# Kernel tuning notes

Measured on AMD Instinct MI355X. Metric: run time of the kernel, lower is better.

## Reference

```python
import jax, jax.numpy as jnp
import numpy as np


def _conv(x, w):
    # 'same'-padded NCHW conv, stride 1, no bias (matches nn.Conv2d(..., padding=k//2, bias=False))
    return jax.lax.conv_general_dilated(x, w, (1, 1), 'SAME',
                                        dimension_numbers=('NCHW', 'OIHW', 'NCHW'))


def setup_inputs() -> dict:
    key = jax.random.key(0)
    ks = jax.random.split(key, 11)
    b, C, H, W = 8, 64, 192, 192
    n_classes, n_space = 2, 8
    return {
        'x': jax.random.normal(ks[0], (b, C, H, W), jnp.float32),
        'class_score': jax.random.normal(ks[1], (b, n_classes, H, W), jnp.float32),
        # to_cspace: Conv2d(1, n_space-1, 3, padding=1)
        'W_cspace': jax.random.normal(ks[2], (n_space - 1, 1, 3, 3), jnp.float32) * 0.1,
        # to_xspace: Conv2d(C, C*n_space, 3, padding=1)
        'W_xspace': jax.random.normal(ks[3], (C * n_space, C, 3, 3), jnp.float32) * 0.02,
        # 1x1 convs stored as squeezed vectors (no bias)
        'W_combine_space': jax.random.normal(ks[4], (n_space,), jnp.float32) * 0.3,  # Conv2d(n_space,1,1)
        'W_cvalue': jax.random.normal(ks[5], (n_space,), jnp.float32) * 0.3,        # Conv2d(1,n_space,1)
        'W_attn': jax.random.normal(ks[6], (n_space,), jnp.float32) * 0.3,          # Conv2d(1,n_space,1)
        'W_combine': jax.random.normal(ks[7], (n_space,), jnp.float32) * 0.3,       # Conv2d(n_space,1,1)
        # single_conv: Conv2d(C,C,3) + BatchNorm2d(C) + ReLU
        'W_single': jax.random.normal(ks[8], (C, C, 3, 3), jnp.float32) * 0.02,
        'bn_gamma': jnp.ones((C,), jnp.float32),
        'bn_beta': jnp.zeros((C,), jnp.float32),
    }


def reference(x, class_score, W_cspace, W_xspace, W_combine_space, W_cvalue,
              W_attn, W_combine, W_single, bn_gamma, bn_beta):
    b, C, H, Wd = x.shape
    nc = class_score.shape[1]           # n_classes
    s = W_cvalue.shape[0]               # n_space
    class_prob = jax.nn.sigmoid(class_score)                       # (b, c, H, W)

    # per-class spatial 'spaces'
    space0 = class_prob.reshape(b * nc, 1, H, Wd)                  # (b*c, 1, H, W)
    space = jnp.concatenate([space0, jax.nn.sigmoid(_conv(space0, W_cspace))], axis=1)  # (b*c, s, H, W)
    space_norm = space / jnp.sum(space, axis=(2, 3), keepdims=True)
    space_norm = space_norm.reshape(b, nc, s, H, Wd).transpose(0, 2, 1, 3, 4)  # (b, s, c, H, W)

    # project x into s spaces, then contract over spatial dims (replaces broadcast-mul + double sum)
    xv = _conv(x, W_xspace).reshape(b, s, C, H, Wd)                # (b, s, d, H, W)
    tok = jnp.einsum('bsdhw,bschw->bscd', xv, space_norm)          # (b, s, c, d)
    tok = jnp.einsum('s,bscd->bcd', W_combine_space, tok)          # combine_space 1x1 conv -> (b, c, d)

    # class value / attention (1x1 convs over a singleton channel == broadcast scale)
    cval = tok[:, None] * W_cvalue[None, :, None, None]            # (b, s, c, d)
    attn = class_prob.reshape(b, nc, H * Wd).transpose(0, 2, 1)    # (b, hw, c)
    attn = jax.nn.sigmoid(attn[:, None] * W_attn[None, :, None, None])  # (b, s, hw, c)

    # attention matmul + combine 1x1 conv fused into one contraction (linear ops commute)
    info = jnp.einsum('s,bsnc,bscd->bnd', W_combine, attn, cval)   # (b, hw, d)
    info = info.transpose(0, 2, 1).reshape(b, C, H, Wd)            # (b, d, H, W)

    # single_conv: conv3x3 -> BatchNorm2d (training-mode batch stats, biased var) -> ReLU
    y = _conv(info, W_single)
    mean = jnp.mean(y, axis=(0, 2, 3), keepdims=True)
    var = jnp.var(y, axis=(0, 2, 3), keepdims=True)
    y = jax.nn.relu((y - mean) * jax.lax.rsqrt(var + 1e-5)
                    * bn_gamma[None, :, None, None] + bn_beta[None, :, None, None])
    return x + y
```

## Files before the change

### kernel.cpp

```cpp
#include <hip/hip_runtime.h>
#include <math.h>

#define B   8
#define C   64
#define HH  192
#define WWD 192
#define P   (HH*WWD)
#define NC  2
#define NS  8
#define PP  (194*194)

#define OFF_SPACE 0
#define OFF_WT    0
#define OFF_GM    294912
#define OFF_SPART 4817408
#define OFF_R     4835840
#define OFF_TOK2  4909568
#define OFF_U     4910592
#define OFF_STP   4919808
#define OFF_SCALE 4956672
#define OFF_SHIFT 4956736
#define WS_FLOATS 4956800

__device__ __forceinline__ float sigm(float x) { return 1.0f / (1.0f + expf(-x)); }

__global__ void k_space(const float* __restrict__ cs, const float* __restrict__ Wc,
                        float* __restrict__ spp, float* __restrict__ Spart) {
    int m = blockIdx.y;
    int bx = blockIdx.x;
    int p = bx * 256 + threadIdx.x;
    int h = p / WWD, w = p - (p / WWD) * WWD;
    float cp[9];
    #pragma unroll
    for (int ky = 0; ky < 3; ky++)
        #pragma unroll
        for (int kx = 0; kx < 3; kx++) {
            int hh = h + ky - 1, ww = w + kx - 1;
            float v = 0.f;
            if ((unsigned)hh < HH && (unsigned)ww < WWD)
                v = sigm(cs[m * P + hh * WWD + ww]);
            cp[ky * 3 + kx] = v;
        }
    float ch[8];
    ch[0] = cp[4];
    #pragma unroll
    for (int j = 0; j < 7; j++) {
        float a = 0.f;
        #pragma unroll
        for (int k = 0; k < 9; k++) a += Wc[j * 9 + k] * cp[k];
        ch[j + 1] = sigm(a);
    }
    #pragma unroll
    for (int q = 0; q < 8; q++)
        spp[(m * 8 + q) * PP + (h + 1) * 194 + (w + 1)] = ch[q];
    __shared__ float red[4][8];
    int lane = threadIdx.x & 63, wave = threadIdx.x >> 6;
    #pragma unroll
    for (int q = 0; q < 8; q++) {
        float v = ch[q];
        for (int off = 32; off > 0; off >>= 1) v += __shfl_down(v, off);
        if (lane == 0) red[wave][q] = v;
    }
    __syncthreads();
    if (threadIdx.x < 8) {
        int q = threadIdx.x;
        Spart[(m * 8 + q) * 144 + bx] = red[0][q] + red[1][q] + red[2][q] + red[3][q];
    }
}

__launch_bounds__(256, 3)
__global__ void k_R2(const float* __restrict__ x, const float* __restrict__ spp,
                     float* __restrict__ R) {
    int ig = blockIdx.x;
    int scz = blockIdx.y;
    int b  = blockIdx.z;
    int sc = scz & 15;
    int half = scz >> 4;
    int s = sc >> 1, c = sc & 1;
    const float* xb = x + (b * C + ig * 8) * P;
    const float* sp = spp + ((b * NC + c) * NS + s) * PP;

    float acc[8][9];
    #pragma unroll
    for (int i = 0; i < 8; i++)
        #pragma unroll
        for (int t = 0; t < 9; t++) acc[i][t] = 0.f;

    for (int it = half * 18; it < half * 18 + 18; it++) {
        int p0 = it * 1024 + threadIdx.x * 4;
        int h = p0 / WWD, w0 = p0 - (p0 / WWD) * WWD;
        float4 xv[8];
        #pragma unroll
        for (int i = 0; i < 8; i++) xv[i] = *(const float4*)(xb + i * P + p0);
        float g[3][6];
        #pragma unroll
        for (int ty = 0; ty < 3; ty++) {
            const float* rp = sp + (h + 2 - ty) * 194 + w0;
            float4 ga; float2 gb;
            __builtin_memcpy(&ga, rp, 16);
            __builtin_memcpy(&gb, rp + 4, 8);
            g[ty][0] = ga.x; g[ty][1] = ga.y; g[ty][2] = ga.z;
            g[ty][3] = ga.w; g[ty][4] = gb.x; g[ty][5] = gb.y;
        }
        #pragma unroll
        for (int ty = 0; ty < 3; ty++)
            #pragma unroll
            for (int tx = 0; tx < 3; tx++) {
                float g0 = g[ty][2 - tx], g1 = g[ty][3 - tx];
                float g2 = g[ty][4 - tx], g3 = g[ty][5 - tx];
                #pragma unroll
                for (int i = 0; i < 8; i++) {
                    float a = acc[i][ty * 3 + tx];
                    a += xv[i].x * g0; a += xv[i].y * g1;
                    a += xv[i].z * g2; a += xv[i].w * g3;
                    acc[i][ty * 3 + tx] = a;
                }
            }
    }

    __shared__ float red[4][72];
    int lane = threadIdx.x & 63, wave = threadIdx.x >> 6;
    #pragma unroll
    for (int i = 0; i < 8; i++)
        #pragma unroll
        for (int t = 0; t < 9; t++) {
            float v = acc[i][t];
            for (int off = 32; off > 0; off >>= 1) v += __shfl_down(v, off);
            if (lane == 0) red[wave][i * 9 + t] = v;
        }
    __syncthreads();
    if (threadIdx.x < 72) {
        int i = threadIdx.x / 9, t = threadIdx.x - (threadIdx.x / 9) * 9;
        float v = red[0][threadIdx.x] + red[1][threadIdx.x] +
                  red[2][threadIdx.x] + red[3][threadIdx.x];
        atomicAdd(&R[((b * 16 + sc) * 64 + (ig * 8 + i)) * 9 + t], v);
    }
}

__global__ void k_wt(const float* __restrict__ Wxs, float* __restrict__ Wt) {
    int t = blockIdx.x;
    int s = blockIdx.y;
    int d = threadIdx.x;
    Wt[(s * 576 + t) * 64 + d] = Wxs[(s * 64 + d) * 576 + t];
}

__global__ void k_g(const float* __restrict__ cs, const float* __restrict__ Wcval,
                    const float* __restrict__ Wattn, const float* __restrict__ Wcomb,
                    float* __restrict__ gmap) {
    int m = blockIdx.y;
    int p = blockIdx.x * 256 + threadIdx.x;
    float wa[8], wt[8];
    #pragma unroll
    for (int s = 0; s < 8; s++) { wa[s] = Wcomb[s] * Wcval[s]; wt[s] = Wattn[s]; }
    float cp = sigm(cs[m * P + p]);
    float a = 0.f;
    #pragma unroll
    for (int s = 0; s < 8; s++) a += wa[s] * sigm(cp * wt[s]);
    gmap[m * P + p] = a;
}

__global__ void k_tok2(const float* __restrict__ Wt, const float* __restrict__ Wcs,
                       const float* __restrict__ R, const float* __restrict__ Spart,
                       float* __restrict__ tok2) {
    int bc = blockIdx.x, s = blockIdx.y;
    int d = threadIdx.x;
    const float* spp = Spart + (bc * 8 + s) * 144;
    float sv = 0.f;
    for (int k = d; k < 144; k += 64) sv += spp[k];
    #pragma unroll
    for (int msk = 32; msk >= 1; msk >>= 1) sv += __shfl_xor(sv, msk);

    const float* Rp = R + ((bc & 1) + ((bc >> 1) * 16 + s * 2)) * 576;
    const float* Wp = Wt + s * 576 * 64 + d;
    float a = 0.f;
    #pragma unroll 4
    for (int t = 0; t < 576; t++) a += Wp[t * 64] * Rp[t];
    float val = a * Wcs[s] / sv;
    atomicAdd(&tok2[bc * C + d], val);
}

__global__ void k_U(const float* __restrict__ Ws, const float* __restrict__ tok2,
                    float* __restrict__ U) {
    int b = blockIdx.x, m = blockIdx.y, oc = threadIdx.x;
    const float* tp = tok2 + (b * NC + m) * C;
    float u[9];
    #pragma unroll
    for (int t = 0; t < 9; t++) u[t] = 0.f;
    for (int ci = 0; ci < C; ci++) {
        float tv = tp[ci];
        const float* wp = Ws + (oc * C + ci) * 9;
        #pragma unroll
        for (int t = 0; t < 9; t++) u[t] += wp[t] * tv;
    }
    float* up = U + ((b * C + oc) * 2 + m) * 9;
    #pragma unroll
    for (int t = 0; t < 9; t++) up[t] = u[t];
}

__device__ __forceinline__ void stage_g(const float* __restrict__ gmap, int b, int ty0, int tx0,
                                        float* h0, float* h1) {
    const float* g0p = gmap + (b * NC + 0) * P;
    const float* g1p = gmap + (b * NC + 1) * P;
    for (int idx = threadIdx.x; idx < 34 * 34; idx += 256) {
        int i = idx / 34, j = idx - (idx / 34) * 34;
        int gy = ty0 - 1 + i, gx = tx0 - 1 + j;
        float a0 = 0.f, a1 = 0.f;
        if ((unsigned)gy < HH && (unsigned)gx < WWD) {
            int p = gy * WWD + gx;
            a0 = g0p[p]; a1 = g1p[p];
        }
        h0[i * 35 + j] = a0; h1[i * 35 + j] = a1;
    }
}

__launch_bounds__(256)
__global__ void k_cs(const float* __restrict__ gmap, const float* __restrict__ U,
                     float* __restrict__ STp) {
    int tile = blockIdx.x, ocg = blockIdx.y, b = blockIdx.z;
    int ty0 = (tile / 6) * 32, tx0 = (tile % 6) * 32;
    __shared__ float h0[34 * 35], h1[34 * 35];
    stage_g(gmap, b, ty0, tx0, h0, h1);
    __syncthreads();

    int w = __builtin_amdgcn_readfirstlane(threadIdx.x >> 6);
    int lane = threadIdx.x & 63;
    int oc0 = ocg * 8 + w * 2;
    float u0[2][9], u1[2][9];
    #pragma unroll
    for (int j = 0; j < 2; j++) {
        const float* up = U + ((b * C + oc0 + j) * 2) * 9;
        #pragma unroll
        for (int t = 0; t < 9; t++) { u0[j][t] = up[t]; u1[j][t] = up[9 + t]; }
    }
    float s1[2] = {0.f, 0.f}, s2[2] = {0.f, 0.f};
    for (int it = 0; it < 4; it++) {
        int row = it * 8 + (lane >> 3);
        int c0 = (lane & 7) * 4;
        float g0v[3][6], g1v[3][6];
        #pragma unroll
        for (int dy = 0; dy < 3; dy++)
            #pragma unroll
            for (int dx = 0; dx < 6; dx++) {
                g0v[dy][dx] = h0[(row + dy) * 35 + c0 + dx];
                g1v[dy][dx] = h1[(row + dy) * 35 + c0 + dx];
            }
        #pragma unroll
        for (int j = 0; j < 2; j++)
            #pragma unroll
            for (int px = 0; px < 4; px++) {
                float y = 0.f;
                #pragma unroll
                for (int ky = 0; ky < 3; ky++)
                    #pragma unroll
                    for (int kx = 0; kx < 3; kx++) {
                        y += u0[j][ky * 3 + kx] * g0v[ky][px + kx];
                        y += u1[j][ky * 3 + kx] * g1v[ky][px + kx];
                    }
                s1[j] += y; s2[j] += y * y;
            }
    }
    #pragma unroll
    for (int j = 0; j < 2; j++) {
        float a = s1[j], q = s2[j];
        for (int off = 32; off > 0; off >>= 1) { a += __shfl_down(a, off); q += __shfl_down(q, off); }
        if (lane == 0) {
            int slot = b * 36 + tile;
            STp[slot * 64 + (oc0 + j)] = a;
            STp[288 * 64 + slot * 64 + (oc0 + j)] = q;
        }
    }
}

__global__ void k_bnfin(const float* __restrict__ STp, const float* __restrict__ gamma,
                        const float* __restrict__ beta, float* __restrict__ scale,
                        float* __restrict__ shift) {
    int oc = threadIdx.x;
    double s = 0.0, s2 = 0.0;
    for (int k = 0; k < 288; k++) {
        s  += (double)STp[k * 64 + oc];
        s2 += (double)STp[288 * 64 + k * 64 + oc];
    }
    double n = (double)(B * P);
    double mean = s / n;
    double var = s2 / n - mean * mean;
    float sc = gamma[oc] * rsqrtf((float)var + 1e-5f);
    scale[oc] = sc;
    shift[oc] = beta[oc] - (float)mean * sc;
}

__launch_bounds__(256)
__global__ void k_fin2(const float* __restrict__ gmap, const float* __restrict__ U,
                       const float* __restrict__ x,
                       const float* __restrict__ scale, const float* __restrict__ shift,
                       float* __restrict__ out) {
    int tile = blockIdx.x, ocg = blockIdx.y, b = blockIdx.z;
    int ty0 = (tile / 6) * 32, tx0 = (tile % 6) * 32;
    __shared__ float h0[34 * 35], h1[34 * 35];
    stage_g(gmap, b, ty0, tx0, h0, h1);
    __syncthreads();

    int w = __builtin_amdgcn_readfirstlane(threadIdx.x >> 6);
    int lane = threadIdx.x & 63;
    int oc0 = ocg * 8 + w * 2;
    float u0[2][9], u1[2][9], sc[2], sh[2];
    #pragma unroll
    for (int j = 0; j < 2; j++) {
        const float* up = U + ((b * C + oc0 + j) * 2) * 9;
        #pragma unroll
        for (int t = 0; t < 9; t++) { u0[j][t] = up[t]; u1[j][t] = up[9 + t]; }
        sc[j] = scale[oc0 + j]; sh[j] = shift[oc0 + j];
    }
    for (int it = 0; it < 4; it++) {
        int row = it * 8 + (lane >> 3);
        int c0 = (lane & 7) * 4;
        float g0v[3][6], g1v[3][6];
        #pragma unroll
        for (int dy = 0; dy < 3; dy++)
            #pragma unroll
            for (int dx = 0; dx < 6; dx++) {
                g0v[dy][dx] = h0[(row + dy) * 35 + c0 + dx];
                g1v[dy][dx] = h1[(row + dy) * 35 + c0 + dx];
            }
        #pragma unroll
        for (int j = 0; j < 2; j++) {
            float y4[4];
            #pragma unroll
            for (int px = 0; px < 4; px++) {
                float y = 0.f;
                #pragma unroll
                for (int ky = 0; ky < 3; ky++)
                    #pragma unroll
                    for (int kx = 0; kx < 3; kx++) {
                        y += u0[j][ky * 3 + kx] * g0v[ky][px + kx];
                        y += u1[j][ky * 3 + kx] * g1v[ky][px + kx];
                    }
                y4[px] = y;
            }
            int ga = (b * C + oc0 + j) * P + (ty0 + row) * WWD + tx0 + c0;
            float4 xv = *(const float4*)(x + ga);
            float4 ov;
            ov.x = fmaxf(y4[0] * sc[j] + sh[j], 0.f) + xv.x;
            ov.y = fmaxf(y4[1] * sc[j] + sh[j], 0.f) + xv.y;
            ov.z = fmaxf(y4[2] * sc[j] + sh[j], 0.f) + xv.z;
            ov.w = fmaxf(y4[3] * sc[j] + sh[j], 0.f) + xv.w;
            *(float4*)(out + ga) = ov;
        }
    }
}

extern "C" void kernel_launch(void* const* d_in, const int* in_sizes, int n_in,
                              void* d_out, int out_size, void* d_ws, size_t ws_size,
                              hipStream_t stream) {
    const float* x     = (const float*)d_in[0];
    const float* cs    = (const float*)d_in[1];
    const float* Wc    = (const float*)d_in[2];
    const float* Wxs   = (const float*)d_in[3];
    const float* Wcsp  = (const float*)d_in[4];
    const float* Wcval = (const float*)d_in[5];
    const float* Wattn = (const float*)d_in[6];
    const float* Wcomb = (const float*)d_in[7];
    const float* Wsing = (const float*)d_in[8];
    const float* gamma = (const float*)d_in[9];
    const float* beta  = (const float*)d_in[10];
    float* ws  = (float*)d_ws;
    float* out = (float*)d_out;

    float* spp   = ws + OFF_SPACE;
    float* Wt    = ws + OFF_WT;
    float* gmap  = ws + OFF_GM;
    float* Spart = ws + OFF_SPART;
    float* R     = ws + OFF_R;
    float* tok2  = ws + OFF_TOK2;
    float* U     = ws + OFF_U;
    float* STp   = ws + OFF_STP;
    float* scale = ws + OFF_SCALE;
    float* shift = ws + OFF_SHIFT;

    hipMemsetAsync(ws, 0, (size_t)(OFF_TOK2 + 1024) * sizeof(float), stream);

    k_space<<<dim3(144, 16), 256, 0, stream>>>(cs, Wc, spp, Spart);
    k_R2   <<<dim3(8, 32, 8), 256, 0, stream>>>(x, spp, R);
    k_wt   <<<dim3(576, 8), 64, 0, stream>>>(Wxs, Wt);
    k_g    <<<dim3(144, 16), 256, 0, stream>>>(cs, Wcval, Wattn, Wcomb, gmap);
    k_tok2 <<<dim3(16, 8), 64, 0, stream>>>(Wt, Wcsp, R, Spart, tok2);
    k_U    <<<dim3(8, 2), 64, 0, stream>>>(Wsing, tok2, U);
    k_cs   <<<dim3(36, 8, 8), 256, 0, stream>>>(gmap, U, STp);
    k_bnfin<<<1, 64, 0, stream>>>(STp, gamma, beta, scale, shift);
    k_fin2 <<<dim3(36, 8, 8), 256, 0, stream>>>(gmap, U, x, scale, shift, out);
}
```

Baseline: 426.6 us.

## Restructure k_R2 so each block covers all space-class pairs, sharing x through shuffles

k_R2 previously launched one block per (space,class) pair and half-range, so each block re-read the 8 x channels from global memory for every one of the 16 pairs. Now each block takes a pixel chunk and a channel group. Its 16-lane subgroups each handle one (space,class) pair, and the x values are loaded once per wave and spread across lanes with __shfl, which cuts redundant global reads of x. The block-level shared-memory reduction becomes a 16-lane shuffle reduction followed by more atomics, and launch bounds rise to 4 blocks per SM. In exchange, every FMA group now costs extra shuffle instructions and more atomics are issued.

```diff
diff --git a/kernel.cpp b/kernel.cpp
--- a/kernel.cpp
+++ b/kernel.cpp
@@ -68,14 +68,17 @@
     }
 }
 
-__launch_bounds__(256, 3)
+__launch_bounds__(256, 4)
 __global__ void k_R2(const float* __restrict__ x, const float* __restrict__ spp,
                      float* __restrict__ R) {
-    int ig = blockIdx.x;
-    int scz = blockIdx.y;
-    int b  = blockIdx.z;
-    int sc = scz & 15;
-    int half = scz >> 4;
+    int ks = blockIdx.x;
+    int bz = blockIdx.y;
+    int b = bz >> 3, ig = bz & 7;
+    int lane = threadIdx.x & 63;
+    int wv   = threadIdx.x >> 6;
+    int pl   = lane & 15;
+    int scs  = lane >> 4;
+    int sc   = wv * 4 + scs;
     int s = sc >> 1, c = sc & 1;
     const float* xb = x + (b * C + ig * 8) * P;
     const float* sp = spp + ((b * NC + c) * NS + s) * PP;
@@ -86,12 +89,12 @@
         #pragma unroll
         for (int t = 0; t < 9; t++) acc[i][t] = 0.f;
 
-    for (int it = half * 18; it < half * 18 + 18; it++) {
-        int p0 = it * 1024 + threadIdx.x * 4;
+    const int chunk = ks * 2304;
+    for (int it = 0; it < 36; it++) {
+        int p0 = chunk + it * 64 + pl * 4;
+        float4 xl0 = *(const float4*)(xb + scs * P + p0);
+        float4 xl1 = *(const float4*)(xb + (scs + 4) * P + p0);
         int h = p0 / WWD, w0 = p0 - (p0 / WWD) * WWD;
-        float4 xv[8];
-        #pragma unroll
-        for (int i = 0; i < 8; i++) xv[i] = *(const float4*)(xb + i * P + p0);
         float g[3][6];
         #pragma unroll
         for (int ty = 0; ty < 3; ty++) {
@@ -103,38 +106,37 @@
             g[ty][3] = ga.w; g[ty][4] = gb.x; g[ty][5] = gb.y;
         }
         #pragma unroll
-        for (int ty = 0; ty < 3; ty++)
-            #pragma unroll
-            for (int tx = 0; tx < 3; tx++) {
-                float g0 = g[ty][2 - tx], g1 = g[ty][3 - tx];
-                float g2 = g[ty][4 - tx], g3 = g[ty][5 - tx];
+        for (int ch = 0; ch < 8; ch++) {
+            int src = ((ch & 3) << 4) | pl;
+            float4 q;
+            if (ch < 4) q = xl0; else q = xl1;
+            float4 xv;
+            xv.x = __shfl(q.x, src); xv.y = __shfl(q.y, src);
+            xv.z = __shfl(q.z, src); xv.w = __shfl(q.w, src);
+            #pragma unroll
+            for (int ty = 0; ty < 3; ty++)
                 #pragma unroll
-                for (int i = 0; i < 8; i++) {
-                    float a = acc[i][ty * 3 + tx];
-                    a += xv[i].x * g0; a += xv[i].y * g1;
-                    a += xv[i].z * g2; a += xv[i].w * g3;
-                    acc[i][ty * 3 + tx] = a;
+                for (int tx = 0; tx < 3; tx++) {
+                    float a = acc[ch][ty * 3 + tx];
+                    a += xv.x * g[ty][2 - tx]; a += xv.y * g[ty][3 - tx];
+                    a += xv.z * g[ty][4 - tx]; a += xv.w * g[ty][5 - tx];
+                    acc[ch][ty * 3 + tx] = a;
                 }
-            }
-    }
-
-    __shared__ float red[4][72];
-    int lane = threadIdx.x & 63, wave = threadIdx.x >> 6;
-    #pragma unroll
-    for (int i = 0; i < 8; i++)
+        }
+    }
+
+    #pragma unroll
+    for (int ch = 0; ch < 8; ch++)
         #pragma unroll
         for (int t = 0; t < 9; t++) {
-            float v = acc[i][t];
-            for (int off = 32; off > 0; off >>= 1) v += __shfl_down(v, off);
-            if (lane == 0) red[wave][i * 9 + t] = v;
-        }
-    __syncthreads();
-    if (threadIdx.x < 72) {
-        int i = threadIdx.x / 9, t = threadIdx.x - (threadIdx.x / 9) * 9;
-        float v = red[0][threadIdx.x] + red[1][threadIdx.x] +
-                  red[2][threadIdx.x] + red[3][threadIdx.x];
-        atomicAdd(&R[((b * 16 + sc) * 64 + (ig * 8 + i)) * 9 + t], v);
-    }
+            float v = acc[ch][t];
+            v += __shfl_down(v, 8, 16);
+            v += __shfl_down(v, 4, 16);
+            v += __shfl_down(v, 2, 16);
+            v += __shfl_down(v, 1, 16);
+            if (pl == 0)
+                atomicAdd(&R[((b * 16 + sc) * 64 + (ig * 8 + ch)) * 9 + t], v);
+        }
 }
 
 __global__ void k_wt(const float* __restrict__ Wxs, float* __restrict__ Wt) {
@@ -379,7 +381,7 @@
     hipMemsetAsync(ws, 0, (size_t)(OFF_TOK2 + 1024) * sizeof(float), stream);
 
     k_space<<<dim3(144, 16), 256, 0, stream>>>(cs, Wc, spp, Spart);
-    k_R2   <<<dim3(8, 32, 8), 256, 0, stream>>>(x, spp, R);
+    k_R2   <<<dim3(16, 64), 256, 0, stream>>>(x, spp, R);
     k_wt   <<<dim3(576, 8), 64, 0, stream>>>(Wxs, Wt);
     k_g    <<<dim3(144, 16), 256, 0, stream>>>(cs, Wcval, Wattn, Wcomb, gmap);
     k_tok2 <<<dim3(16, 8), 64, 0, stream>>>(Wt, Wcsp, R, Spart, tok2);
```

New measurement: 887.1 us. +107.9%, slower.

## Stage x tiles in shared memory and share them across four space-class waves

Applied to the files above, without the earlier changes.

Reworks k_R2 so each block loads an 8-channel x tile into LDS once and four waves, each handling a different (space, class) pair, reuse it. Before, every block streamed x from global memory separately for each of 16 sc combinations; now x global traffic drops about fourfold. Pixel work is split into 4 chunks instead of 2, and the cross-wave LDS reduction is replaced by per-wave atomics. The cost is two barriers per tile, more atomics, and LDS pressure that may reduce occupancy.

```diff
diff --git a/kernel.cpp b/kernel.cpp
--- a/kernel.cpp
+++ b/kernel.cpp
@@ -71,70 +71,76 @@
 __launch_bounds__(256, 3)
 __global__ void k_R2(const float* __restrict__ x, const float* __restrict__ spp,
                      float* __restrict__ R) {
-    int ig = blockIdx.x;
-    int scz = blockIdx.y;
-    int b  = blockIdx.z;
-    int sc = scz & 15;
-    int half = scz >> 4;
+    int mq = blockIdx.x;
+    int bz = blockIdx.y;
+    int ks = blockIdx.z;
+    int b = bz >> 3, ig = bz & 7;
+    int tid = threadIdx.x;
+    int wv = tid >> 6, lane = tid & 63;
+    int sc = mq * 4 + wv;
     int s = sc >> 1, c = sc & 1;
     const float* xb = x + (b * C + ig * 8) * P;
     const float* sp = spp + ((b * NC + c) * NS + s) * PP;
 
+    __shared__ float xt[8][1024];
+
     float acc[8][9];
     #pragma unroll
     for (int i = 0; i < 8; i++)
         #pragma unroll
         for (int t = 0; t < 9; t++) acc[i][t] = 0.f;
 
-    for (int it = half * 18; it < half * 18 + 18; it++) {
-        int p0 = it * 1024 + threadIdx.x * 4;
-        int h = p0 / WWD, w0 = p0 - (p0 / WWD) * WWD;
-        float4 xv[8];
-        #pragma unroll
-        for (int i = 0; i < 8; i++) xv[i] = *(const float4*)(xb + i * P + p0);
-        float g[3][6];
-        #pragma unroll
-        for (int ty = 0; ty < 3; ty++) {
-            const float* rp = sp + (h + 2 - ty) * 194 + w0;
-            float4 ga; float2 gb;
-            __builtin_memcpy(&ga, rp, 16);
-            __builtin_memcpy(&gb, rp + 4, 8);
-            g[ty][0] = ga.x; g[ty][1] = ga.y; g[ty][2] = ga.z;
-            g[ty][3] = ga.w; g[ty][4] = gb.x; g[ty][5] = gb.y;
-        }
-        #pragma unroll
-        for (int ty = 0; ty < 3; ty++)
-            #pragma unroll
-            for (int tx = 0; tx < 3; tx++) {
-                float g0 = g[ty][2 - tx], g1 = g[ty][3 - tx];
-                float g2 = g[ty][4 - tx], g3 = g[ty][5 - tx];
+    for (int t9 = 0; t9 < 9; t9++) {
+        int tile = (ks * 9 + t9) * 1024;
+        {
+            int px = tid * 4;
+            #pragma unroll
+            for (int i = 0; i < 8; i++) {
+                float4 v = *(const float4*)(xb + i * P + tile + px);
+                *(float4*)(&xt[i][px]) = v;
+            }
+        }
+        __syncthreads();
+        for (int sub = 0; sub < 4; sub++) {
+            int lpx = sub * 256 + lane * 4;
+            int p0 = tile + lpx;
+            int h = p0 / WWD, w0 = p0 - (p0 / WWD) * WWD;
+            float g[3][6];
+            #pragma unroll
+            for (int ty = 0; ty < 3; ty++) {
+                const float* rp = sp + (h + 2 - ty) * 194 + w0;
+                float4 ga; float2 gb;
+                __builtin_memcpy(&ga, rp, 16);
+                __builtin_memcpy(&gb, rp + 4, 8);
+                g[ty][0] = ga.x; g[ty][1] = ga.y; g[ty][2] = ga.z;
+                g[ty][3] = ga.w; g[ty][4] = gb.x; g[ty][5] = gb.y;
+            }
+            #pragma unroll
+            for (int i = 0; i < 8; i++) {
+                float4 xv = *(const float4*)(&xt[i][lpx]);
                 #pragma unroll
-                for (int i = 0; i < 8; i++) {
-                    float a = acc[i][ty * 3 + tx];
-                    a += xv[i].x * g0; a += xv[i].y * g1;
-                    a += xv[i].z * g2; a += xv[i].w * g3;
-                    acc[i][ty * 3 + tx] = a;
-                }
-            }
-    }
-
-    __shared__ float red[4][72];
-    int lane = threadIdx.x & 63, wave = threadIdx.x >> 6;
+                for (int ty = 0; ty < 3; ty++)
+                    #pragma unroll
+                    for (int tx = 0; tx < 3; tx++) {
+                        float a = acc[i][ty * 3 + tx];
+                        a += xv.x * g[ty][2 - tx]; a += xv.y * g[ty][3 - tx];
+                        a += xv.z * g[ty][4 - tx]; a += xv.w * g[ty][5 - tx];
+                        acc[i][ty * 3 + tx] = a;
+                    }
+            }
+        }
+        __syncthreads();
+    }
+
     #pragma unroll
     for (int i = 0; i < 8; i++)
         #pragma unroll
         for (int t = 0; t < 9; t++) {
             float v = acc[i][t];
             for (int off = 32; off > 0; off >>= 1) v += __shfl_down(v, off);
-            if (lane == 0) red[wave][i * 9 + t] = v;
-        }
-    __syncthreads();
-    if (threadIdx.x < 72) {
-        int i = threadIdx.x / 9, t = threadIdx.x - (threadIdx.x / 9) * 9;
-        float v = red[0][threadIdx.x] + red[1][threadIdx.x] +
-                  red[2][threadIdx.x] + red[3][threadIdx.x];
-        atomicAdd(&R[((b * 16 + sc) * 64 + (ig * 8 + i)) * 9 + t], v);
-    }
+            if (lane == 0)
+                atomicAdd(&R[((b * 16 + sc) * 64 + (ig * 8 + i)) * 9 + t], v);
+        }
 }
 
 __global__ void k_wt(const float* __restrict__ Wxs, float* __restrict__ Wt) {
@@ -379,7 +385,7 @@
     hipMemsetAsync(ws, 0, (size_t)(OFF_TOK2 + 1024) * sizeof(float), stream);
 
     k_space<<<dim3(144, 16), 256, 0, stream>>>(cs, Wc, spp, Spart);
-    k_R2   <<<dim3(8, 32, 8), 256, 0, stream>>>(x, spp, R);
+    k_R2   <<<dim3(4, 64, 4), 256, 0, stream>>>(x, spp, R);
     k_wt   <<<dim3(576, 8), 64, 0, stream>>>(Wxs, Wt);
     k_g    <<<dim3(144, 16), 256, 0, stream>>>(cs, Wcval, Wattn, Wcomb, gmap);
     k_tok2 <<<dim3(16, 8), 64, 0, stream>>>(Wt, Wcsp, R, Spart, tok2);
```

After: 578.6 us. 1.36x slower.
